# Optimization experiments

Hardware: AMD Instinct MI355X
Metric: run time of the kernel (lower is better)

Reference implementation:

```python
import jax, jax.numpy as jnp
import numpy as np

N_NODES = 50000
N_EDGES = 600000
N_FEAT = 256
N_HID = 128
N_CLASS = 64
HEADS = 8
LEAKY_SLOPE = 0.2


def setup_inputs() -> dict:
    key = jax.random.key(0)
    ks = jax.random.split(key, 12)
    D0 = N_HID // HEADS  # 16 per-head dim, layer 0
    x = jax.random.normal(ks[0], (N_NODES, N_FEAT), dtype=jnp.float32)
    edge_index = jax.random.randint(ks[1], (2, N_EDGES), 0, N_NODES, dtype=jnp.int64)
    s0 = 1.0 / np.sqrt(N_FEAT)
    s1 = 1.0 / np.sqrt(N_HID)
    return {
        "x": x,
        "edge_index": edge_index,
        "W0": jax.random.normal(ks[2], (N_FEAT, HEADS * D0), dtype=jnp.float32) * s0,
        "a_src0": jax.random.normal(ks[3], (HEADS, D0), dtype=jnp.float32) * s0,
        "a_dst0": jax.random.normal(ks[4], (HEADS, D0), dtype=jnp.float32) * s0,
        "b0": jnp.zeros((HEADS * D0,), dtype=jnp.float32),
        "W1": jax.random.normal(ks[5], (N_HID, HEADS * N_CLASS), dtype=jnp.float32) * s1,
        "a_src1": jax.random.normal(ks[6], (HEADS, N_CLASS), dtype=jnp.float32) * s1,
        "a_dst1": jax.random.normal(ks[7], (HEADS, N_CLASS), dtype=jnp.float32) * s1,
        "b1": jnp.zeros((N_CLASS,), dtype=jnp.float32),
    }


def gat_conv(x, src, dst, W, a_s, a_d, b, concat, num_nodes):
    H, D = a_s.shape
    h = (x @ W).reshape(-1, H, D)                    # [N, H, D]
    alpha_s = jnp.einsum('nhd,hd->nh', h, a_s)       # [N, H]
    alpha_d = jnp.einsum('nhd,hd->nh', h, a_d)       # [N, H]
    e = jax.nn.leaky_relu(alpha_s[src] + alpha_d[dst], LEAKY_SLOPE)  # [E, H]
    # numerically stable edge-softmax grouped by destination node
    m = jax.ops.segment_max(e, dst, num_segments=num_nodes)
    m = jnp.where(jnp.isfinite(m), m, 0.0)           # nodes with no in-edges
    ex = jnp.exp(e - m[dst])
    denom = jax.ops.segment_sum(ex, dst, num_segments=num_nodes)
    alpha = ex / (denom[dst] + 1e-16)                # [E, H]
    msg = h[src] * alpha[:, :, None]                 # [E, H, D]
    out = jax.ops.segment_sum(msg, dst, num_segments=num_nodes)  # [N, H, D]
    if concat:
        out = out.reshape(num_nodes, H * D)
    else:
        out = out.mean(axis=1)
    return out + b


def reference(x, edge_index, W0, a_src0, a_dst0, b0, W1, a_src1, a_dst1, b1):
    src, dst = edge_index[0], edge_index[1]
    h = gat_conv(x, src, dst, W0, a_src0, a_dst0, b0, True, N_NODES)
    h = jax.nn.elu(h)  # eval mode: dropout is identity
    h = gat_conv(h, src, dst, W1, a_src1, a_dst1, b1, False, N_NODES)
    return jax.nn.log_softmax(h, axis=-1)
```

## Files before the change

kernel.cpp:

```cpp
#include <hip/hip_runtime.h>
#include <hip/hip_bf16.h>
#include <math.h>

#define NN 50000
#define NE 600000
#define NF 256
#define NHID 128
#define HEADS 8
#define D0 16
#define NCLS 64
#define NB1 196

#define PK0 (9 * 8 * 64 * 8)
#define PK1 (4 * 32 * 64 * 8)
#define PKA (4 * 64 * 8)
#define CASTN (NN * NF / 4)
#define PREPN (PK0 + PK1 + PKA)

typedef __attribute__((ext_vector_type(8))) short short8;
typedef __attribute__((ext_vector_type(4))) float floatx4;

__device__ __forceinline__ float bf16lo(uint v) { return __uint_as_float((v & 0xffffu) << 16); }
__device__ __forceinline__ float bf16hi(uint v) { return __uint_as_float(v & 0xffff0000u); }
__device__ __forceinline__ uint packbf16(float a, float b) {
    return (uint)__bfloat16_as_ushort(__float2bfloat16(a)) |
           ((uint)__bfloat16_as_ushort(__float2bfloat16(b)) << 16);
}
__device__ __forceinline__ short f2bf(float v) {
    return (short)__bfloat16_as_ushort(__float2bfloat16(v));
}
__device__ __forceinline__ float bf16tof(short v) {
    return __uint_as_float(((uint)(ushort)v) << 16);
}


__global__ void scan1_kernel(const int* __restrict__ deg, int* __restrict__ rs,
                             int* __restrict__ bsum) {
    __shared__ int sh[256];
    int tid = threadIdx.x;
    int i = blockIdx.x * 256 + tid;
    int v = (i < NN) ? deg[i] : 0;
    sh[tid] = v;
    __syncthreads();
    for (int off = 1; off < 256; off <<= 1) {
        int t = (tid >= off) ? sh[tid - off] : 0;
        __syncthreads();
        sh[tid] += t;
        __syncthreads();
    }
    if (i < NN) rs[i] = sh[tid] - v;
    if (tid == 255) bsum[blockIdx.x] = sh[255];
}

__global__ void scan2_kernel(const int* __restrict__ bsum, int* __restrict__ bsumx) {
    __shared__ int sh[256];
    int tid = threadIdx.x;
    int v = (tid < NB1) ? bsum[tid] : 0;
    sh[tid] = v;
    __syncthreads();
    for (int off = 1; off < 256; off <<= 1) {
        int t = (tid >= off) ? sh[tid - off] : 0;
        __syncthreads();
        sh[tid] += t;
        __syncthreads();
    }
    if (tid < NB1) bsumx[tid] = sh[tid] - v;
}

__global__ void scan3_kernel(int* __restrict__ rs, const int* __restrict__ bsumx) {
    int i = blockIdx.x * 256 + threadIdx.x;
    if (i < NN) rs[i] += bsumx[i >> 8];
}

__global__ void scatter_kernel(const int* __restrict__ ei, const int* __restrict__ rs,
                               int* __restrict__ cnt2, int* __restrict__ csr) {
    int e = blockIdx.x * 256 + threadIdx.x;
    if (e >= NE) return;
    int s = ei[e], d = ei[NE + e];
    int pos = rs[d] + atomicAdd(&cnt2[d], 1);
    csr[pos] = s;
}


__global__ void fused_prep_kernel(const float* __restrict__ x, short* __restrict__ xb,
                                  const int* __restrict__ ei, int* __restrict__ deg,
                                  const float* __restrict__ W0, const float* __restrict__ aS0,
                                  const float* __restrict__ aD0, const float* __restrict__ W1,
                                  const float* __restrict__ aS1, const float* __restrict__ aD1,
                                  short* __restrict__ Bp0, short* __restrict__ Bp1,
                                  short* __restrict__ wA1b) {
    int i = blockIdx.x * 256 + threadIdx.x;
    if (i < CASTN) {
        float4 v = ((const float4*)x)[i];
        short4 r;
        r.x = f2bf(v.x); r.y = f2bf(v.y); r.z = f2bf(v.z); r.w = f2bf(v.w);
        ((short4*)xb)[i] = r;
        return;
    }
    int e = i - CASTN;
    if (e < NE) {
        atomicAdd(&deg[ei[NE + e]], 1);
        return;
    }
    int tid = e - NE;
    if (tid < PK0) {
        int j = tid & 7, l = (tid >> 3) & 63, ks = (tid >> 9) & 7, t = tid >> 12;
        int k = ks * 32 + (l >> 4) * 8 + j;
        float v;
        if (t < 8) {
            int c = t * 16 + (l & 15);
            v = W0[(size_t)k * 128 + c];
        } else {
            int jj = l & 15;
            int hh = jj & 7;
            const float* av = (jj < 8) ? aS0 : aD0;
            float sum = 0.f;
            for (int dd = 0; dd < D0; ++dd)
                sum += W0[(size_t)k * 128 + hh * D0 + dd] * av[hh * D0 + dd];
            v = sum;
        }
        Bp0[tid] = f2bf(v);
    } else if (tid < PK0 + PK1) {
        int t2 = tid - PK0;
        int j = t2 & 7, l = (t2 >> 3) & 63, ks = (t2 >> 9) & 31, t = t2 >> 14;
        int kk = ks * 32 + (l >> 4) * 8 + j;
        int c = t * 16 + (l & 15);
        Bp1[t2] = f2bf(W1[(size_t)(kk & 127) * 512 + (kk >> 7) * 64 + c] * 0.125f);
    } else if (tid < PREPN) {
        int t3 = tid - PK0 - PK1;
        int j = t3 & 7, l = (t3 >> 3) & 63, ks = t3 >> 9;
        int k = ks * 32 + (l >> 4) * 8 + j;
        int c = l & 15;
        int h = c & 7;
        const float* av = (c < 8) ? aS1 : aD1;
        float sum = 0.f;
        for (int d2 = 0; d2 < NCLS; ++d2)
            sum += W1[(size_t)k * 512 + h * NCLS + d2] * av[h * NCLS + d2];
        wA1b[t3] = f2bf(sum);
    }
}


__global__ __launch_bounds__(256) void gemm0_mfma(const short* __restrict__ xb,
                                                  const short* __restrict__ Bp,
                                                  ushort* __restrict__ h0b,
                                                  float* __restrict__ as0,
                                                  float* __restrict__ ad0) {
    int lane = threadIdx.x & 63, wave = threadIdx.x >> 6;
    int rg = wave >> 1, cg = wave & 1;
    int q = lane >> 4, c16 = lane & 15;
    int row0 = blockIdx.x * 32 + rg * 16;
    int arow = row0 + c16;
    if (arow > NN - 1) arow = NN - 1;
    const short* ap = xb + (size_t)arow * NF + q * 8;
    floatx4 acc[5] = {};
#pragma unroll
    for (int ks = 0; ks < 8; ++ks) {
        short8 af = *(const short8*)(ap + ks * 32);
#pragma unroll
        for (int tt = 0; tt < 4; ++tt) {
            int t = cg * 4 + tt;
            short8 bf = *(const short8*)(Bp + (((size_t)t * 8 + ks) * 64 + lane) * 8);
            acc[tt] = __builtin_amdgcn_mfma_f32_16x16x32_bf16(af, bf, acc[tt], 0, 0, 0);
        }
        if (cg) {
            short8 bf = *(const short8*)(Bp + (((size_t)8 * 8 + ks) * 64 + lane) * 8);
            acc[4] = __builtin_amdgcn_mfma_f32_16x16x32_bf16(af, bf, acc[4], 0, 0, 0);
        }
    }
#pragma unroll
    for (int r = 0; r < 4; ++r) {
        int grow = row0 + q * 4 + r;
        if (grow >= NN) continue;
#pragma unroll
        for (int tt = 0; tt < 4; ++tt)
            h0b[(size_t)grow * NHID + cg * 64 + tt * 16 + c16] =
                (ushort)f2bf(acc[tt][r]);
        if (cg) {
            float v = acc[4][r];
            if (c16 < 8) as0[grow * 8 + c16] = v;
            else         ad0[grow * 8 + (c16 - 8)] = v;
        }
    }
}

__global__ __launch_bounds__(256) void alpha1_mfma(const ushort* __restrict__ x1b,
                                                   const short* __restrict__ wA1b,
                                                   float* __restrict__ as1,
                                                   float* __restrict__ ad1) {
    int lane = threadIdx.x & 63, wave = threadIdx.x >> 6;
    int q = lane >> 4, c16 = lane & 15;
    int row0 = blockIdx.x * 64 + wave * 16;
    int arow = row0 + c16;
    if (arow > NN - 1) arow = NN - 1;
    const short* ap = (const short*)x1b + (size_t)arow * NHID + q * 8;
    floatx4 acc = {};
#pragma unroll
    for (int ks = 0; ks < 4; ++ks) {
        short8 af = *(const short8*)(ap + ks * 32);
        short8 bf = *(const short8*)(wA1b + (((size_t)ks) * 64 + lane) * 8);
        acc = __builtin_amdgcn_mfma_f32_16x16x32_bf16(af, bf, acc, 0, 0, 0);
    }
#pragma unroll
    for (int r = 0; r < 4; ++r) {
        int grow = row0 + q * 4 + r;
        if (grow >= NN) continue;
        float v = acc[r];
        if (c16 < 8) as1[grow * 8 + c16] = v;
        else         ad1[grow * 8 + (c16 - 8)] = v;
    }
}


__global__ __launch_bounds__(256) void fused_edge0(
    const int* __restrict__ rs, const int* __restrict__ deg, const int* __restrict__ csr,
    const ushort* __restrict__ h0b, const float* __restrict__ as0, const float* __restrict__ ad0,
    const float* __restrict__ b0, ushort* __restrict__ x1b) {
    int d = (blockIdx.x * 256 + threadIdx.x) >> 6;
    int lane = threadIdx.x & 63;
    if (d >= NN) return;
    int row = rs[d], dg = deg[d];
    int hl = lane & 7, g = lane >> 3;
    int hp = lane >> 3;
    float adv = ad0[d * 8 + hl];
    float den = 0.f;
    float2 acc = {0.f, 0.f};
    for (int base = 0; base < dg; base += 8) {
        int i = base + g;
        int s = (i < dg) ? csr[row + i] : 0;
        float ev = as0[s * 8 + hl] + adv;
        ev = ev > 0.f ? ev : 0.2f * ev;
        float p = (i < dg) ? __expf(ev) : 0.f;
        den += p;
        uint vbuf[8];
#pragma unroll
        for (int g2 = 0; g2 < 8; ++g2) {
            int sg = __builtin_amdgcn_readlane(s, g2 * 8);
            vbuf[g2] = *(const uint*)(h0b + (size_t)sg * NHID + 2 * lane);
        }
#pragma unroll
        for (int g2 = 0; g2 < 8; ++g2) {
            float ph = __shfl(p, g2 * 8 + hp);
            acc.x += bf16lo(vbuf[g2]) * ph;
            acc.y += bf16hi(vbuf[g2]) * ph;
        }
    }
    den += __shfl_xor(den, 8);
    den += __shfl_xor(den, 16);
    den += __shfl_xor(den, 32);
    float dh = __shfl(den, hp);
    float inv = 1.f / (dh + 1e-16f);
    float2 bb = ((const float2*)b0)[lane];
    float o0 = acc.x * inv + bb.x;
    float o1 = acc.y * inv + bb.y;
    o0 = o0 > 0.f ? o0 : expf(o0) - 1.f;
    o1 = o1 > 0.f ? o1 : expf(o1) - 1.f;
    *(uint*)(x1b + (size_t)d * NHID + 2 * lane) = packbf16(o0, o1);
}

__global__ __launch_bounds__(256) void fused_edge1(
    const int* __restrict__ rs, const int* __restrict__ deg, const int* __restrict__ csr,
    const ushort* __restrict__ x1b, const float* __restrict__ as1, const float* __restrict__ ad1,
    const short* __restrict__ Bp1, const float* __restrict__ b1, float* __restrict__ out) {
    __shared__ ushort aggNsh[4][2][1024];
    int gw = (blockIdx.x * 256 + threadIdx.x) >> 6;
    int wave = threadIdx.x >> 6;
    int lane = threadIdx.x & 63;
    int dA = 2 * gw;
    if (dA >= NN) return;
    int dB = dA + 1;
    int q = lane >> 4, c16 = lane & 15, h7 = lane & 7;
    int d_l = (lane >= 32) ? dB : dA;
    int row_l = rs[d_l], dg_l = deg[d_l];
    bool V = ((lane & 8) == 0) == (lane < 32);
    float adv = ad1[d_l * 8 + h7];
    int dgA = __shfl(dg_l, 0);
    int dgB = __shfl(dg_l, 32);
    int dgmax = dgA > dgB ? dgA : dgB;
    float den = 0.f;
    floatx4 acc[8] = {};
    for (int base = 0; base < dgmax; base += 16) {
        short8 af;
        int sarr[8];
#pragma unroll
        for (int j = 0; j < 8; ++j) {
            int idx = base + (q & 1) * 8 + j;
            int s = 0;
            if (idx < dg_l) s = csr[row_l + idx];
            sarr[j] = s;
            float ev = as1[s * 8 + h7] + adv;
            ev = ev > 0.f ? ev : 0.2f * ev;
            float p = __expf(ev);
            p = (idx < dg_l && V) ? p : 0.f;
            short pb = f2bf(p);
            af[j] = pb;
            den += bf16tof(pb);
        }
#pragma unroll
        for (int t = 0; t < 8; ++t) {
            short8 bv;
#pragma unroll
            for (int j = 0; j < 8; ++j)
                bv[j] = (short)x1b[(size_t)sarr[j] * NHID + t * 16 + c16];
            acc[t] = __builtin_amdgcn_mfma_f32_16x16x32_bf16(af, bv, acc[t], 0, 0, 0);
        }
    }
    den += __shfl_xor(den, 8);
    den += __shfl_xor(den, 16);
    int hbase = (q & 1) * 4;
    int drow = lane >> 5;
#pragma unroll
    for (int r = 0; r < 4; ++r) {
        int hh = hbase + r;
        float dh = __shfl(den, (lane & 32) + hh);
        float inv = 1.f / (dh + 1e-16f);
#pragma unroll
        for (int t = 0; t < 8; ++t)
            aggNsh[wave][drow][hh * 128 + t * 16 + c16] = (ushort)f2bf(acc[t][r] * inv);
    }
    asm volatile("" ::: "memory");
    int rsel = c16 & 1;
    const short* abase = (const short*)&aggNsh[wave][rsel][q * 8];
    floatx4 acc2[4] = {};
    for (int ks = 0; ks < 32; ++ks) {
        short8 af2 = *(const short8*)(abase + ks * 32);
#pragma unroll
        for (int t = 0; t < 4; ++t) {
            short8 bf = *(const short8*)(Bp1 + (((size_t)t * 32 + ks) * 64 + lane) * 8);
            acc2[t] = __builtin_amdgcn_mfma_f32_16x16x32_bf16(af2, bf, acc2[t], 0, 0, 0);
        }
    }
    float bias2[4];
#pragma unroll
    for (int t = 0; t < 4; ++t) bias2[t] = b1[t * 16 + c16];
#pragma unroll
    for (int r2 = 0; r2 < 2; ++r2) {
        int dd = (r2 == 0) ? dA : dB;
        float z[4];
        float mx = -INFINITY;
#pragma unroll
        for (int t = 0; t < 4; ++t) {
            z[t] = acc2[t][r2] + bias2[t];
            mx = fmaxf(mx, z[t]);
        }
        mx = fmaxf(mx, __shfl_xor(mx, 1));
        mx = fmaxf(mx, __shfl_xor(mx, 2));
        mx = fmaxf(mx, __shfl_xor(mx, 4));
        mx = fmaxf(mx, __shfl_xor(mx, 8));
        float s = 0.f;
#pragma unroll
        for (int t = 0; t < 4; ++t) s += expf(z[t] - mx);
        s += __shfl_xor(s, 1);
        s += __shfl_xor(s, 2);
        s += __shfl_xor(s, 4);
        s += __shfl_xor(s, 8);
        float lse = mx + logf(s);
        if (q == 0) {
#pragma unroll
            for (int t = 0; t < 4; ++t)
                out[(size_t)dd * NCLS + t * 16 + c16] = z[t] - lse;
        }
    }
}


extern "C" void kernel_launch(void* const* d_in, const int* in_sizes, int n_in,
                              void* d_out, int out_size, void* d_ws, size_t ws_size,
                              hipStream_t stream) {
    const float* x   = (const float*)d_in[0];
    const int*   ei  = (const int*)d_in[1];
    const float* W0  = (const float*)d_in[2];
    const float* aS0 = (const float*)d_in[3];
    const float* aD0 = (const float*)d_in[4];
    const float* b0  = (const float*)d_in[5];
    const float* W1  = (const float*)d_in[6];
    const float* aS1 = (const float*)d_in[7];
    const float* aD1 = (const float*)d_in[8];
    const float* b1  = (const float*)d_in[9];
    float* out = (float*)d_out;

    char* ws = (char*)d_ws;
    ushort* x1b = (ushort*)ws; ws += (size_t)NN * NHID * 2;
    ushort* h0b = (ushort*)ws; ws += (size_t)NN * NHID * 2;
    short* xb   = (short*)ws; ws += (size_t)NN * NF * 2;
    float* as0  = (float*)ws; ws += (size_t)NN * HEADS * 4;
    float* ad0  = (float*)ws; ws += (size_t)NN * HEADS * 4;
    float* as1  = (float*)ws; ws += (size_t)NN * HEADS * 4;
    float* ad1  = (float*)ws; ws += (size_t)NN * HEADS * 4;
    short* Bp0  = (short*)ws; ws += (size_t)PK0 * 2;
    short* Bp1  = (short*)ws; ws += (size_t)PK1 * 2;
    short* wA1b = (short*)ws; ws += (size_t)PKA * 2;
    int* deg    = (int*)ws; ws += (size_t)NN * 4;
    int* cnt2   = (int*)ws; ws += (size_t)NN * 4;
    int* rs     = (int*)ws; ws += (size_t)NN * 4;
    int* bsum   = (int*)ws; ws += 256 * 4;
    int* bsumx  = (int*)ws; ws += 256 * 4;
    int* csr    = (int*)ws; ws += (size_t)NE * 4;

    const int FUSEDN = CASTN + NE + PREPN;

    hipMemsetAsync(deg, 0, (size_t)2 * NN * 4, stream);
    fused_prep_kernel<<<(FUSEDN + 255) / 256, 256, 0, stream>>>(
        x, xb, ei, deg, W0, aS0, aD0, W1, aS1, aD1, Bp0, Bp1, wA1b);

    scan1_kernel<<<NB1, 256, 0, stream>>>(deg, rs, bsum);
    scan2_kernel<<<1, 256, 0, stream>>>(bsum, bsumx);
    scan3_kernel<<<NB1, 256, 0, stream>>>(rs, bsumx);
    scatter_kernel<<<(NE + 255) / 256, 256, 0, stream>>>(ei, rs, cnt2, csr);

    gemm0_mfma<<<(NN + 31) / 32, 256, 0, stream>>>(xb, Bp0, h0b, as0, ad0);
    fused_edge0<<<(NN + 3) / 4, 256, 0, stream>>>(rs, deg, csr, h0b, as0, ad0, b0, x1b);

    alpha1_mfma<<<(NN + 63) / 64, 256, 0, stream>>>(x1b, wA1b, as1, ad1);
    fused_edge1<<<(NN / 2 + 3) / 4, 256, 0, stream>>>(rs, deg, csr, x1b, as1, ad1,
                                                      Bp1, b1, out);
}
```

Measured before the change: 366.6 us.

## Split layer-1 output GEMM across waves with K-partitioned block reduction

In the second edge kernel, each wave used to run the full 1024-deep projection GEMM for its own two nodes, using only 2 of the 16 MFMA rows. Now the block's 8 nodes share LDS rows. Each wave computes a K-slice of 8 steps for all 8 nodes, writes partial results to shared memory, and after a block barrier each wave reduces the partials and performs log-softmax across 64 lanes. This cuts the redundant Bp1 weight loads and MFMA count by 4x, at the cost of two __syncthreads and extra LDS traffic.

```diff
diff --git a/kernel.cpp b/kernel.cpp
--- a/kernel.cpp
+++ b/kernel.cpp
@@ -262,12 +262,12 @@
     const int* __restrict__ rs, const int* __restrict__ deg, const int* __restrict__ csr,
     const ushort* __restrict__ x1b, const float* __restrict__ as1, const float* __restrict__ ad1,
     const short* __restrict__ Bp1, const float* __restrict__ b1, float* __restrict__ out) {
-    __shared__ ushort aggNsh[4][2][1024];
-    int gw = (blockIdx.x * 256 + threadIdx.x) >> 6;
+    __shared__ ushort aggNsh[8][1032];
+    __shared__ float Csh[4][8][64];
     int wave = threadIdx.x >> 6;
     int lane = threadIdx.x & 63;
+    int gw = blockIdx.x * 4 + wave;
     int dA = 2 * gw;
-    if (dA >= NN) return;
     int dB = dA + 1;
     int q = lane >> 4, c16 = lane & 15, h7 = lane & 7;
     int d_l = (lane >= 32) ? dB : dA;
@@ -308,7 +308,7 @@
     den += __shfl_xor(den, 8);
     den += __shfl_xor(den, 16);
     int hbase = (q & 1) * 4;
-    int drow = lane >> 5;
+    int lrow = wave * 2 + (lane >> 5);
 #pragma unroll
     for (int r = 0; r < 4; ++r) {
         int hh = hbase + r;
@@ -316,51 +316,57 @@
         float inv = 1.f / (dh + 1e-16f);
 #pragma unroll
         for (int t = 0; t < 8; ++t)
-            aggNsh[wave][drow][hh * 128 + t * 16 + c16] = (ushort)f2bf(acc[t][r] * inv);
-    }
-    asm volatile("" ::: "memory");
-    int rsel = c16 & 1;
-    const short* abase = (const short*)&aggNsh[wave][rsel][q * 8];
-    floatx4 acc2[4] = {};
-    for (int ks = 0; ks < 32; ++ks) {
-        short8 af2 = *(const short8*)(abase + ks * 32);
-#pragma unroll
-        for (int t = 0; t < 4; ++t) {
-            short8 bf = *(const short8*)(Bp1 + (((size_t)t * 32 + ks) * 64 + lane) * 8);
-            acc2[t] = __builtin_amdgcn_mfma_f32_16x16x32_bf16(af2, bf, acc2[t], 0, 0, 0);
-        }
-    }
-    float bias2[4];
-#pragma unroll
-    for (int t = 0; t < 4; ++t) bias2[t] = b1[t * 16 + c16];
-#pragma unroll
-    for (int r2 = 0; r2 < 2; ++r2) {
-        int dd = (r2 == 0) ? dA : dB;
-        float z[4];
-        float mx = -INFINITY;
-#pragma unroll
-        for (int t = 0; t < 4; ++t) {
-            z[t] = acc2[t][r2] + bias2[t];
-            mx = fmaxf(mx, z[t]);
-        }
-        mx = fmaxf(mx, __shfl_xor(mx, 1));
-        mx = fmaxf(mx, __shfl_xor(mx, 2));
-        mx = fmaxf(mx, __shfl_xor(mx, 4));
-        mx = fmaxf(mx, __shfl_xor(mx, 8));
-        float s = 0.f;
-#pragma unroll
-        for (int t = 0; t < 4; ++t) s += expf(z[t] - mx);
-        s += __shfl_xor(s, 1);
-        s += __shfl_xor(s, 2);
-        s += __shfl_xor(s, 4);
-        s += __shfl_xor(s, 8);
-        float lse = mx + logf(s);
-        if (q == 0) {
-#pragma unroll
-            for (int t = 0; t < 4; ++t)
-                out[(size_t)dd * NCLS + t * 16 + c16] = z[t] - lse;
-        }
-    }
+            aggNsh[lrow][hh * 128 + t * 16 + c16] = (ushort)f2bf(acc[t][r] * inv);
+    }
+    __syncthreads();
+    {
+        floatx4 acc2[4] = {};
+        const short* abase = (const short*)&aggNsh[c16 & 7][0];
+        int ks0 = wave * 8;
+#pragma unroll
+        for (int kk = 0; kk < 8; ++kk) {
+            int ks = ks0 + kk;
+            short8 af2 = *(const short8*)(abase + ks * 32 + q * 8);
+#pragma unroll
+            for (int t = 0; t < 4; ++t) {
+                short8 bf = *(const short8*)(Bp1 + (((size_t)t * 32 + ks) * 64 + lane) * 8);
+                acc2[t] = __builtin_amdgcn_mfma_f32_16x16x32_bf16(af2, bf, acc2[t], 0, 0, 0);
+            }
+        }
+        if (q < 2) {
+#pragma unroll
+            for (int r = 0; r < 4; ++r)
+#pragma unroll
+                for (int t = 0; t < 4; ++t)
+                    Csh[wave][q * 4 + r][t * 16 + c16] = acc2[t][r];
+        }
+    }
+    __syncthreads();
+    float z0 = 0.f, z1 = 0.f;
+#pragma unroll
+    for (int w2 = 0; w2 < 4; ++w2) {
+        z0 += Csh[w2][wave * 2][lane];
+        z1 += Csh[w2][wave * 2 + 1][lane];
+    }
+    float bb = b1[lane];
+    z0 += bb;
+    z1 += bb;
+    float mx0 = z0, mx1 = z1;
+#pragma unroll
+    for (int x = 1; x < 64; x <<= 1) {
+        mx0 = fmaxf(mx0, __shfl_xor(mx0, x));
+        mx1 = fmaxf(mx1, __shfl_xor(mx1, x));
+    }
+    float s0 = expf(z0 - mx0), s1 = expf(z1 - mx1);
+#pragma unroll
+    for (int x = 1; x < 64; x <<= 1) {
+        s0 += __shfl_xor(s0, x);
+        s1 += __shfl_xor(s1, x);
+    }
+    float lse0 = mx0 + logf(s0);
+    float lse1 = mx1 + logf(s1);
+    out[(size_t)dA * NCLS + lane] = z0 - lse0;
+    out[(size_t)dB * NCLS + lane] = z1 - lse1;
 }
 
 
@@ -412,6 +418,5 @@
     fused_edge0<<<(NN + 3) / 4, 256, 0, stream>>>(rs, deg, csr, h0b, as0, ad0, b0, x1b);
 
     alpha1_mfma<<<(NN + 63) / 64, 256, 0, stream>>>(x1b, wA1b, as1, ad1);
-    fused_edge1<<<(NN / 2 + 3) / 4, 256, 0, stream>>>(rs, deg, csr, x1b, as1, ad1,
-                                                      Bp1, b1, out);
-}
+    fused_edge1<<<NN / 8, 256, 0, stream>>>(rs, deg, csr, x1b, as1, ad1, Bp1, b1, out);
+}
```

Result: faster. 312.7 us (-14.7%).
